# Optimization experiments

Measured on AMD Instinct MI355X. Metric: run time of the kernel, lower is better.

## Reference

```python
import jax, jax.numpy as jnp
import numpy as np

B, D, SL, N, H, LL = 2, 128, 1024, 64, 4, 4
LN_EPS = 1e-5
DIST_EPS = 1e-8


def _ln(x, g, b):
    m = x.mean(-1, keepdims=True)
    v = ((x - m) ** 2).mean(-1, keepdims=True)
    return (x - m) / jnp.sqrt(v + LN_EPS) * g + b


def _sla(x, qw, qb, kw, kb, vw, vb, ow, ob):
    # x: [B, R, C, D]; rank-1 scaled linear attention (head_qk_dim = 1)
    Bq, R, C, Dd = x.shape
    Hh = qw.shape[0]
    hd = Dd // Hh
    q = jnp.einsum('brcd,hd->brhc', x, qw) + qb[:, None]   # [B,R,H,C]
    k = jnp.einsum('brcd,hd->brhc', x, kw) + kb[:, None]
    q = jax.nn.elu(q) + 1.0
    k = jax.nn.elu(k) + 1.0
    q = q / q.mean(-1, keepdims=True)
    k = k / k.sum(-1, keepdims=True)
    v = (jnp.einsum('brcd,ed->brce', x, vw) + vb).reshape(Bq, R, C, Hh, hd)
    v = v.transpose(0, 1, 3, 2, 4)                         # [B,R,H,C,hd]
    ktv = jnp.einsum('brhc,brhce->brhe', k, v)             # [B,R,H,hd]
    V = jnp.einsum('brhc,brhe->brche', q, ktv)             # [B,R,C,H,hd]
    V = V.reshape(Bq, R, C, Dd)
    return jnp.einsum('brcd,ed->brce', V, ow) + ob


def _forward(x, rq_w, rq_b, rk_w, rk_b, rv_w, rv_b, ro_w, ro_b,
             cq_w, cq_b, ck_w, ck_b, cv_w, cv_b, co_w, co_b,
             ln_r_g, ln_r_b, ln_c_g, ln_c_b, ln_f_g, ln_f_b,
             f1_w, f1_b, f2_w, f2_b):
    y = x.transpose(0, 2, 3, 1)   # [B, L, N, D] channels-last

    def layer(y, p):
        (rqw, rqb, rkw, rkb, rvw, rvb, row_, rob,
         cqw, cqb, ckw, ckb, cvw, cvb, cow, cob,
         lrg, lrb, lcg, lcb, lfg, lfb, f1w, f1b, f2w, f2b) = p
        # row attention: rows = L, cols = N
        y = y + _sla(_ln(y, lrg, lrb), rqw, rqb, rkw, rkb, rvw, rvb, row_, rob)
        # col attention: rows = N, cols = L
        hc = _ln(y, lcg, lcb).swapaxes(1, 2)
        y = y + _sla(hc, cqw, cqb, ckw, ckb, cvw, cvb, cow, cob).swapaxes(1, 2)
        # FFN (1x1 convs == pointwise linears)
        hf = _ln(y, lfg, lfb)
        hf = jax.nn.gelu(jnp.einsum('blnd,ed->blne', hf, f1w) + f1b, approximate=False)
        y = y + (jnp.einsum('blne,de->blnd', hf, f2w) + f2b)
        return y, None

    params = (rq_w, rq_b, rk_w, rk_b, rv_w, rv_b, ro_w, ro_b,
              cq_w, cq_b, ck_w, ck_b, cv_w, cv_b, co_w, co_b,
              ln_r_g, ln_r_b, ln_c_g, ln_c_b, ln_f_g, ln_f_b,
              f1_w, f1_b, f2_w, f2_b)
    y, _ = jax.lax.scan(layer, y, params)

    # Euclidean pairwise distance head (use_cls=False): mean over sites 1..L
    xb = y[:, 1:].mean(axis=1)                 # [B, N, D]
    i0, i1 = np.tril_indices(N, -1)            # lower=True, diff=True ordering
    diffs = xb[:, i0] - xb[:, i1]              # [B, n_pairs, D]
    return jnp.sqrt(jnp.sum(diffs * diffs, axis=-1) + DIST_EPS)


def setup_inputs() -> dict:
    key = jax.random.key(0)
    ks = jax.random.split(key, 12)
    s = 0.02
    z = lambda *sh: jnp.zeros(sh, jnp.float32)
    o = lambda *sh: jnp.ones(sh, jnp.float32)
    w = lambda k, sh: jax.random.normal(k, sh, jnp.float32) * s
    p = {'x': jax.random.normal(ks[0], (B, D, SL, N), jnp.float32)}
    p['rq_w'] = w(ks[1], (LL, H, D)); p['rq_b'] = z(LL, H)
    p['rk_w'] = w(ks[2], (LL, H, D)); p['rk_b'] = z(LL, H)
    p['rv_w'] = w(ks[3], (LL, D, D)); p['rv_b'] = z(LL, D)
    p['ro_w'] = w(ks[4], (LL, D, D)); p['ro_b'] = z(LL, D)
    p['cq_w'] = w(ks[5], (LL, H, D)); p['cq_b'] = z(LL, H)
    p['ck_w'] = w(ks[6], (LL, H, D)); p['ck_b'] = z(LL, H)
    p['cv_w'] = w(ks[7], (LL, D, D)); p['cv_b'] = z(LL, D)
    p['co_w'] = w(ks[8], (LL, D, D)); p['co_b'] = z(LL, D)
    p['ln_r_g'] = o(LL, D); p['ln_r_b'] = z(LL, D)
    p['ln_c_g'] = o(LL, D); p['ln_c_b'] = z(LL, D)
    p['ln_f_g'] = o(LL, D); p['ln_f_b'] = z(LL, D)
    p['f1_w'] = w(ks[9], (LL, 4 * D, D)); p['f1_b'] = z(LL, 4 * D)
    p['f2_w'] = w(ks[10], (LL, D, 4 * D)); p['f2_b'] = z(LL, D)
    return p


def reference(x, rq_w, rq_b, rk_w, rk_b, rv_w, rv_b, ro_w, ro_b,
              cq_w, cq_b, ck_w, ck_b, cv_w, cv_b, co_w, co_b,
              ln_r_g, ln_r_b, ln_c_g, ln_c_b, ln_f_g, ln_f_b,
              f1_w, f1_b, f2_w, f2_b):
    return _forward(x, rq_w, rq_b, rk_w, rk_b, rv_w, rv_b, ro_w, ro_b,
                    cq_w, cq_b, ck_w, ck_b, cv_w, cv_b, co_w, co_b,
                    ln_r_g, ln_r_b, ln_c_g, ln_c_b, ln_f_g, ln_f_b,
                    f1_w, f1_b, f2_w, f2_b)
```

## Files before the change

### kernel.cpp

```cpp
#include <hip/hip_runtime.h>
#include <math.h>

#define LCNT 4

typedef float f32x4 __attribute__((ext_vector_type(4)));
typedef short bf16x8 __attribute__((ext_vector_type(8)));
typedef unsigned int u32;

__device__ __forceinline__ ushort bfr(float x){
  unsigned int b = __float_as_uint(x);
  return (ushort)((b + 0x7FFFu + ((b>>16)&1u)) >> 16);
}
__device__ __forceinline__ unsigned int pk2(float a, float b){
  return (unsigned int)bfr(a) | ((unsigned int)bfr(b)<<16);
}
__device__ __forceinline__ float fast_gelu(float v){
  float s = fabsf(v) * 0.70710678118f;
  float t = 1.0f/(1.0f + 0.3275911f*s);
  float p = t*(0.254829592f + t*(-0.284496736f + t*(1.421413741f +
            t*(-1.453152027f + t*1.061405429f))));
  float e = 1.0f - p*__expf(-s*s);
  e = copysignf(e, v);
  return 0.5f*v*(1.0f + e);
}
__device__ __forceinline__ void gl_lds16(const void* g, void* l){
  __builtin_amdgcn_global_load_lds(
      (const __attribute__((address_space(1))) u32*)g,
      (__attribute__((address_space(3))) u32*)l, 16, 0, 0);
}

__global__ __launch_bounds__(256) void k_transpose(const float* __restrict__ x,
                                                   float* __restrict__ y){
  int g = blockIdx.x;
  int b = g >> 10, l = g & 1023;
  __shared__ float sh[128*65];
  for (int idx = threadIdx.x; idx < 128*64; idx += 256){
    int d = idx >> 6, n = idx & 63;
    sh[d*65+n] = x[(((size_t)b*128 + d)*1024 + l)*64 + n];
  }
  __syncthreads();
  for (int idx = threadIdx.x; idx < 128*64; idx += 256){
    int n = idx >> 7, d = idx & 127;
    y[((size_t)g*64 + n)*128 + d] = sh[d*65+n];
  }
}

__global__ __launch_bounds__(256) void k_cvt(const float* __restrict__ src,
                                             ushort* __restrict__ dst, int n4){
  int i = blockIdx.x*256 + threadIdx.x;
  if (i < n4){
    float4 v = ((const float4*)src)[i];
    ushort4 p; p.x=bfr(v.x); p.y=bfr(v.y); p.z=bfr(v.z); p.w=bfr(v.w);
    ((ushort4*)dst)[i] = p;
  }
}

__global__ __launch_bounds__(256) void k_row(
    float* __restrict__ y,
    const float* __restrict__ rqw, const float* __restrict__ rqb,
    const float* __restrict__ rkw, const float* __restrict__ rkb,
    const float* __restrict__ rvw, const float* __restrict__ rvb,
    const float* __restrict__ roW, const float* __restrict__ rob,
    const float* __restrict__ lrg, const float* __restrict__ lrb,
    const float* __restrict__ cqw, const float* __restrict__ cqb,
    const float* __restrict__ ckw, const float* __restrict__ ckb,
    const float* __restrict__ lcg, const float* __restrict__ lcb,
    float2* __restrict__ stats,
    float* __restrict__ qout, float* __restrict__ kout)
{
  int g = blockIdx.x; int b = g>>10, l = g&1023;
  __shared__ float sh_h[64*129];
  __shared__ float sh_w4[2048];
  __shared__ float sh_q[256], sh_k[256];
  __shared__ float sh_hk[512];
  __shared__ float sh_ktv[128];
  __shared__ __align__(16) float sh_P[512];
  int tid = threadIdx.x;
  for (int i = tid; i < 512; i += 256){
    sh_w4[i] = rqw[i]; sh_w4[512+i] = rkw[i];
    sh_w4[1024+i] = cqw[i]; sh_w4[1536+i] = ckw[i];
  }
  int ttk = tid>>2, s4 = tid&3;
  float* yr = y + ((size_t)g*64 + ttk)*128 + s4*32;
  float4 v[8];
  #pragma unroll
  for (int i=0;i<8;i++) v[i] = *(const float4*)(yr + i*4);
  float sum = 0.f;
  #pragma unroll
  for (int i=0;i<8;i++) sum += v[i].x+v[i].y+v[i].z+v[i].w;
  sum += __shfl_xor(sum,1); sum += __shfl_xor(sum,2);
  float mean = sum*(1.0f/128.0f);
  float vs = 0.f;
  #pragma unroll
  for (int i=0;i<8;i++){
    v[i].x-=mean; v[i].y-=mean; v[i].z-=mean; v[i].w-=mean;
    vs += v[i].x*v[i].x+v[i].y*v[i].y+v[i].z*v[i].z+v[i].w*v[i].w;
  }
  vs += __shfl_xor(vs,1); vs += __shfl_xor(vs,2);
  float rstd = rsqrtf(vs*(1.0f/128.0f) + 1e-5f);
  {
    const float* gp = lrg + s4*32; const float* bp = lrb + s4*32;
    float* hrow = &sh_h[ttk*129 + s4*32];
    #pragma unroll
    for (int i=0;i<8;i++){
      float4 g4 = *(const float4*)(gp+i*4);
      float4 b4 = *(const float4*)(bp+i*4);
      hrow[i*4+0]=v[i].x*rstd*g4.x+b4.x;
      hrow[i*4+1]=v[i].y*rstd*g4.y+b4.y;
      hrow[i*4+2]=v[i].z*rstd*g4.z+b4.z;
      hrow[i*4+3]=v[i].w*rstd*g4.w+b4.w;
    }
  }
  __syncthreads();
  int h = tid>>6, n = tid&63;
  {
    float qr = rqb[h], kr = rkb[h];
    const float* qwp = sh_w4 + h*128;
    const float* kwp = sh_w4 + 512 + h*128;
    const float* hp  = sh_h + n*129;
    #pragma unroll 4
    for (int d=0; d<128; d++){ float hv=hp[d]; qr+=hv*qwp[d]; kr+=hv*kwp[d]; }
    qr = qr > 0.f ? qr + 1.f : __expf(qr);
    kr = kr > 0.f ? kr + 1.f : __expf(kr);
    float qs = qr; for (int m=32;m>=1;m>>=1) qs += __shfl_xor(qs, m);
    float ks = kr; for (int m=32;m>=1;m>>=1) ks += __shfl_xor(ks, m);
    sh_q[h*64+n] = qr * (64.f/qs);
    sh_k[h*64+n] = kr * (1.f/ks);
  }
  __syncthreads();
  #pragma unroll
  for (int r=0;r<2;r++){
    int idx = tid + r*256;
    int hh = idx>>7, d = idx&127;
    float acc = 0.f;
    #pragma unroll 4
    for (int nn=0;nn<64;nn++) acc += sh_k[hh*64+nn]*sh_h[nn*129+d];
    sh_hk[hh*128+d] = acc;
  }
  __syncthreads();
  if (tid < 128){
    float acc = rvb[tid];
    const float* vr = rvw + (size_t)tid*128;
    const float* hp2 = sh_hk + (tid>>5)*128;
    #pragma unroll 4
    for (int d=0;d<128;d++) acc += vr[d]*hp2[d];
    sh_ktv[tid] = acc;
  }
  __syncthreads();
  #pragma unroll
  for (int r=0;r<2;r++){
    int idx = tid + r*256;
    int hh = idx>>7, e = idx&127;
    float acc = 0.f;
    const float* orow = roW + (size_t)e*128 + hh*32;
    #pragma unroll 4
    for (int j=0;j<32;j++) acc += orow[j]*sh_ktv[hh*32+j];
    sh_P[hh*128+e] = acc;
  }
  __syncthreads();
  {
    float q0=sh_q[ttk], q1=sh_q[64+ttk], q2=sh_q[128+ttk], q3=sh_q[192+ttk];
    const float4* P4 = (const float4*)sh_P;
    #pragma unroll
    for (int i=0;i<8;i++){
      int d4 = s4*8 + i;
      float4 p0=P4[d4], p1=P4[32+d4], p2=P4[64+d4], p3=P4[96+d4];
      float4 o4=*(const float4*)&rob[s4*32+i*4];
      v[i].x += mean + o4.x + q0*p0.x+q1*p1.x+q2*p2.x+q3*p3.x;
      v[i].y += mean + o4.y + q0*p0.y+q1*p1.y+q2*p2.y+q3*p3.y;
      v[i].z += mean + o4.z + q0*p0.z+q1*p1.z+q2*p2.z+q3*p3.z;
      v[i].w += mean + o4.w + q0*p0.w+q1*p1.w+q2*p2.w+q3*p3.w;
      *(float4*)(yr + i*4) = v[i];
    }
  }
  float sum2 = 0.f;
  #pragma unroll
  for (int i=0;i<8;i++) sum2 += v[i].x+v[i].y+v[i].z+v[i].w;
  sum2 += __shfl_xor(sum2,1); sum2 += __shfl_xor(sum2,2);
  float cmean = sum2*(1.0f/128.0f);
  float cvs = 0.f;
  #pragma unroll
  for (int i=0;i<8;i++){
    v[i].x-=cmean; v[i].y-=cmean; v[i].z-=cmean; v[i].w-=cmean;
    cvs += v[i].x*v[i].x+v[i].y*v[i].y+v[i].z*v[i].z+v[i].w*v[i].w;
  }
  cvs += __shfl_xor(cvs,1); cvs += __shfl_xor(cvs,2);
  float crstd = rsqrtf(cvs*(1.0f/128.0f) + 1e-5f);
  if (s4 == 0) stats[(size_t)g*64 + ttk] = make_float2(cmean, crstd);
  {
    const float* gp = lcg + s4*32; const float* bp = lcb + s4*32;
    float* hrow = &sh_h[ttk*129 + s4*32];
    #pragma unroll
    for (int i=0;i<8;i++){
      float4 g4 = *(const float4*)(gp+i*4);
      float4 b4 = *(const float4*)(bp+i*4);
      hrow[i*4+0]=v[i].x*crstd*g4.x+b4.x;
      hrow[i*4+1]=v[i].y*crstd*g4.y+b4.y;
      hrow[i*4+2]=v[i].z*crstd*g4.z+b4.z;
      hrow[i*4+3]=v[i].w*crstd*g4.w+b4.w;
    }
  }
  __syncthreads();
  {
    float qv = cqb[h], kv = ckb[h];
    const float* qwp = sh_w4 + 1024 + h*128;
    const float* kwp = sh_w4 + 1536 + h*128;
    const float* hp  = sh_h + n*129;
    #pragma unroll 4
    for (int d=0; d<128; d++){ float hv=hp[d]; qv+=hv*qwp[d]; kv+=hv*kwp[d]; }
    qv = qv > 0.f ? qv + 1.f : __expf(qv);
    kv = kv > 0.f ? kv + 1.f : __expf(kv);
    size_t o = (((size_t)b*64 + n)*4 + h)*1024 + l;
    qout[o] = qv; kout[o] = kv;
  }
}

__global__ __launch_bounds__(256) void k_col_sum(const float* __restrict__ qin,
                                                 float* __restrict__ qs){
  int gg = blockIdx.x;
  const float* qp = qin + (size_t)gg*1024;
  float sq = 0.f;
  for (int i = threadIdx.x; i < 1024; i += 256) sq += qp[i];
  for (int m=32;m>=1;m>>=1) sq += __shfl_xor(sq, m);
  __shared__ float aq[4];
  int w = threadIdx.x >> 6;
  if ((threadIdx.x & 63) == 0) aq[w] = sq;
  __syncthreads();
  if (threadIdx.x == 0) qs[gg] = 1024.f/(aq[0]+aq[1]+aq[2]+aq[3]);
}

__global__ __launch_bounds__(256) void k_col_s1(
    const float* __restrict__ y, const float2* __restrict__ stats,
    const float* __restrict__ kin,
    float* __restrict__ s1p, float* __restrict__ Ab, float* __restrict__ Bb)
{
  int gg = blockIdx.x;
  int s = gg & 7, n = (gg>>3) & 63, b = gg>>9;
  int tid = threadIdx.x;
  int li = tid>>7, d = tid&127;
  const float* kp = kin + ((size_t)(b*64+n)*4)*1024;
  float a0=0.f,a1=0.f,a2=0.f,a3=0.f;
  float A0=0.f,A1=0.f,A2=0.f,A3=0.f;
  float B0=0.f,B1=0.f,B2=0.f,B3=0.f;
  for (int j=0;j<64;j++){
    int l = s*128 + 2*j + li;
    size_t t = ((size_t)(b*1024+l)*64+n);
    float2 st = stats[t];
    float w = st.y * y[t*128 + d];
    float rm = st.y*st.x;
    float k0 = kp[l], k1 = kp[1024+l], k2 = kp[2048+l], k3 = kp[3072+l];
    a0 += k0*w; a1 += k1*w; a2 += k2*w; a3 += k3*w;
    A0 += k0; A1 += k1; A2 += k2; A3 += k3;
    B0 += k0*rm; B1 += k1*rm; B2 += k2*rm; B3 += k3*rm;
  }
  __shared__ float shr[512];
  __shared__ float sAB[8];
  if (li == 1){
    shr[0*128+d]=a0; shr[1*128+d]=a1; shr[2*128+d]=a2; shr[3*128+d]=a3;
    if (d==0){ sAB[0]=A0; sAB[1]=A1; sAB[2]=A2; sAB[3]=A3;
               sAB[4]=B0; sAB[5]=B1; sAB[6]=B2; sAB[7]=B3; }
  }
  __syncthreads();
  if (li == 0){
    float* out = s1p + (size_t)gg*512;
    out[0*128+d] = a0 + shr[0*128+d];
    out[1*128+d] = a1 + shr[1*128+d];
    out[2*128+d] = a2 + shr[2*128+d];
    out[3*128+d] = a3 + shr[3*128+d];
    if (d==0){
      Ab[gg*4+0]=A0+sAB[0]; Ab[gg*4+1]=A1+sAB[1];
      Ab[gg*4+2]=A2+sAB[2]; Ab[gg*4+3]=A3+sAB[3];
      Bb[gg*4+0]=B0+sAB[4]; Bb[gg*4+1]=B1+sAB[5];
      Bb[gg*4+2]=B2+sAB[6]; Bb[gg*4+3]=B3+sAB[7];
    }
  }
}

__global__ __launch_bounds__(256) void k_col_ktvP(
    const float* __restrict__ s1p,
    const float* __restrict__ Ab, const float* __restrict__ Bb,
    const float* __restrict__ vw, const float* __restrict__ vb,
    const float* __restrict__ ow, const float* __restrict__ qsn,
    const float* __restrict__ lcg, const float* __restrict__ lcb,
    float* __restrict__ Pout)
{
  int gg = blockIdx.x;
  __shared__ float sh_hk[512];
  __shared__ float sh_ktv[128];
  __shared__ float sh_A[4], sh_B[4];
  int tid = threadIdx.x;
  #pragma unroll
  for (int r = 0; r < 2; r++){
    int idx = tid + r*256;
    float acc = 0.f;
    #pragma unroll
    for (int s = 0; s < 8; s++) acc += s1p[((size_t)gg*8 + s)*512 + idx];
    sh_hk[idx] = acc;
  }
  if (tid < 4){
    float a=0.f, bb=0.f;
    #pragma unroll
    for (int s = 0; s < 8; s++){ a += Ab[(gg*8+s)*4+tid]; bb += Bb[(gg*8+s)*4+tid]; }
    sh_A[tid]=a; sh_B[tid]=bb;
  }
  __syncthreads();
  #pragma unroll
  for (int r = 0; r < 2; r++){
    int idx = tid + r*256;
    int h = idx>>7, d = idx&127;
    float Ah = sh_A[h];
    sh_hk[idx] = lcg[d]*((sh_hk[idx]-sh_B[h])/Ah) + lcb[d];
  }
  __syncthreads();
  if (tid < 128){
    float acc = vb[tid];
    const float* vr = vw + (size_t)tid*128;
    const float* hp2 = sh_hk + (tid>>5)*128;
    #pragma unroll 4
    for (int d = 0; d < 128; d++) acc += vr[d]*hp2[d];
    sh_ktv[tid] = acc;
  }
  __syncthreads();
  #pragma unroll
  for (int r = 0; r < 2; r++){
    int idx = tid + r*256;
    int hh = idx >> 7, e = idx & 127;
    float acc = 0.f;
    const float* orow = ow + (size_t)e*128 + hh*32;
    #pragma unroll 4
    for (int j = 0; j < 32; j++) acc += orow[j]*sh_ktv[hh*32+j];
    Pout[(size_t)gg*512 + hh*128 + e] = acc * qsn[gg*4 + hh];
  }
}

__global__ __launch_bounds__(512, 4) void k_ffn(
    float* __restrict__ y,
    const float* __restrict__ qbuf, const float* __restrict__ Pb,
    const float* __restrict__ cob,
    const float* __restrict__ gam, const float* __restrict__ bet,
    const ushort* __restrict__ w1b, const float* __restrict__ b1,
    const ushort* __restrict__ w2b, const float* __restrict__ b2)
{
  __shared__ __align__(16) ushort pool[29952];
  ushort* sW1 = pool;
  ushort* sW2 = pool + 8192;
  ushort* sH  = pool + 16384;
  ushort* sHf = pool + 25088;
  float*  sF  = (float*)pool;
  int tid = threadIdx.x;
  int g = blockIdx.x; int b = g>>10, l = g&1023;
  size_t tb = (size_t)g*64;

  int wid = tid>>6, ln = tid&63;
  int lr = ln&15, gq = ln>>4;
  int wt = wid>>1, we = wid&1;
  int t0 = wt*16;

  #pragma unroll
  for (int i = 0; i < 2; i++){
    int row = wid*8 + i*4 + (ln>>4);
    gl_lds16(w1b + (size_t)row*128 + (((ln&15) ^ (row&7))<<3),
             &sW1[(wid*8 + i*4)*128]);
  }
  #pragma unroll
  for (int i = 0; i < 2; i++){
    int row = wid*16 + i*8 + (ln>>3);
    gl_lds16(w2b + (size_t)row*512 + (((ln&7) ^ (row&7))<<3),
             &sW2[(wid*16 + i*8)*64]);
  }

  int ttk = tid>>3, s8 = tid&7;
  float* yr = y + (tb+ttk)*128 + s8*16;
  float4 v[4];
  float fmean;
  {
    #pragma unroll
    for (int i = 0; i < 4; i++) v[i] = *(const float4*)(yr + i*4);
    const float* qp = qbuf + ((size_t)(b*64+ttk)*4)*1024 + l;
    float q0 = qp[0], q1 = qp[1024], q2 = qp[2048], q3 = qp[3072];
    const float* pr = Pb + (size_t)(b*64+ttk)*512 + s8*16;
    #pragma unroll
    for (int i = 0; i < 4; i++){
      float4 p0 = *(const float4*)(pr + i*4);
      float4 p1 = *(const float4*)(pr + 128 + i*4);
      float4 p2 = *(const float4*)(pr + 256 + i*4);
      float4 p3 = *(const float4*)(pr + 384 + i*4);
      float4 c4 = *(const float4*)&cob[s8*16 + i*4];
      v[i].x += c4.x + q0*p0.x+q1*p1.x+q2*p2.x+q3*p3.x;
      v[i].y += c4.y + q0*p0.y+q1*p1.y+q2*p2.y+q3*p3.y;
      v[i].z += c4.z + q0*p0.z+q1*p1.z+q2*p2.z+q3*p3.z;
      v[i].w += c4.w + q0*p0.w+q1*p1.w+q2*p2.w+q3*p3.w;
    }
    float sum = 0.f;
    #pragma unroll
    for (int i = 0; i < 4; i++) sum += v[i].x+v[i].y+v[i].z+v[i].w;
    sum += __shfl_xor(sum,1); sum += __shfl_xor(sum,2); sum += __shfl_xor(sum,4);
    fmean = sum*(1.0f/128.0f);
    float vs = 0.f;
    #pragma unroll
    for (int i = 0; i < 4; i++){
      v[i].x-=fmean; v[i].y-=fmean; v[i].z-=fmean; v[i].w-=fmean;
      vs += v[i].x*v[i].x+v[i].y*v[i].y+v[i].z*v[i].z+v[i].w*v[i].w;
    }
    vs += __shfl_xor(vs,1); vs += __shfl_xor(vs,2); vs += __shfl_xor(vs,4);
    float rstd = rsqrtf(vs*(1.0f/128.0f) + 1e-5f);
    const float* gp = gam + s8*16; const float* bp = bet + s8*16;
    #pragma unroll
    for (int i = 0; i < 2; i++){
      float4 ga = *(const float4*)(gp + i*8),     gb = *(const float4*)(gp + i*8 + 4);
      float4 ba = *(const float4*)(bp + i*8),     bb = *(const float4*)(bp + i*8 + 4);
      float4 va = v[i*2], vb2 = v[i*2+1];
      int4 o;
      o.x = (int)pk2(va.x*rstd*ga.x+ba.x,  va.y*rstd*ga.y+ba.y);
      o.y = (int)pk2(va.z*rstd*ga.z+ba.z,  va.w*rstd*ga.w+ba.w);
      o.z = (int)pk2(vb2.x*rstd*gb.x+bb.x, vb2.y*rstd*gb.y+bb.y);
      o.w = (int)pk2(vb2.z*rstd*gb.z+bb.z, vb2.w*rstd*gb.w+bb.w);
      *(int4*)&sH[ttk*136 + s8*16 + i*8] = o;
    }
  }
  __syncthreads();

  f32x4 acc2[4] = {};

  for (int c = 0; c < 8; c++){
    f32x4 acc1[2] = {};
    #pragma unroll
    for (int ks = 0; ks < 4; ks++){
      bf16x8 bfv = *(const bf16x8*)&sH[(t0+lr)*136 + ks*32 + gq*8];
      #pragma unroll
      for (int i = 0; i < 2; i++){
        int er = we*32 + i*16 + lr;
        bf16x8 afv = *(const bf16x8*)&sW1[er*128 + ((((ks<<2)|gq) ^ (lr&7))<<3)];
        acc1[i] = __builtin_amdgcn_mfma_f32_16x16x32_bf16(afv, bfv, acc1[i], 0, 0, 0);
      }
    }
    #pragma unroll
    for (int i = 0; i < 2; i++){
      float4 bb = *(const float4*)&b1[c*64 + we*32 + i*16 + gq*4];
      ushort4 pk;
      pk.x = bfr(fast_gelu(acc1[i][0] + bb.x));
      pk.y = bfr(fast_gelu(acc1[i][1] + bb.y));
      pk.z = bfr(fast_gelu(acc1[i][2] + bb.z));
      pk.w = bfr(fast_gelu(acc1[i][3] + bb.w));
      *(ushort4*)&sHf[(t0+lr)*72 + we*32 + i*16 + gq*4] = pk;
    }
    __syncthreads();
    if (c < 7){
      #pragma unroll
      for (int i = 0; i < 2; i++){
        int row = wid*8 + i*4 + (ln>>4);
        gl_lds16(w1b + (size_t)(c+1)*8192 + (size_t)row*128 + (((ln&15) ^ (row&7))<<3),
                 &sW1[(wid*8 + i*4)*128]);
      }
    }
    #pragma unroll
    for (int ks = 0; ks < 2; ks++){
      bf16x8 bfv = *(const bf16x8*)&sHf[(t0+lr)*72 + ks*32 + gq*8];
      #pragma unroll
      for (int j = 0; j < 4; j++){
        int dr = we*64 + j*16 + lr;
        bf16x8 afv = *(const bf16x8*)&sW2[dr*64 + ((((ks<<2)|gq) ^ (lr&7))<<3)];
        acc2[j] = __builtin_amdgcn_mfma_f32_16x16x32_bf16(afv, bfv, acc2[j], 0, 0, 0);
      }
    }
    __syncthreads();
    if (c < 7){
      #pragma unroll
      for (int i = 0; i < 2; i++){
        int row = wid*16 + i*8 + (ln>>3);
        gl_lds16(w2b + (size_t)row*512 + (c+1)*64 + (((ln&7) ^ (row&7))<<3),
                 &sW2[(wid*16 + i*8)*64]);
      }
    }
  }

  #pragma unroll
  for (int j = 0; j < 4; j++){
    float4 fo; fo.x=acc2[j][0]; fo.y=acc2[j][1]; fo.z=acc2[j][2]; fo.w=acc2[j][3];
    *(float4*)&sF[(t0+lr)*132 + we*64 + j*16 + gq*4] = fo;
  }
  __syncthreads();
  #pragma unroll
  for (int i = 0; i < 4; i++){
    float4 f = *(const float4*)&sF[ttk*132 + s8*16 + i*4];
    float4 b4 = *(const float4*)&b2[s8*16 + i*4];
    float4 o;
    o.x = v[i].x + fmean + f.x + b4.x;
    o.y = v[i].y + fmean + f.y + b4.y;
    o.z = v[i].z + fmean + f.z + b4.z;
    o.w = v[i].w + fmean + f.w + b4.w;
    *(float4*)(yr + i*4) = o;
  }
}

__global__ __launch_bounds__(128) void k_xbp(const float* __restrict__ y,
                                             float* __restrict__ xbq){
  int gg = blockIdx.x;
  int s = gg & 3, n = (gg>>2) & 63, b = gg>>8;
  int d = threadIdx.x;
  float acc = 0.f;
  int l0 = s*256 + (s==0 ? 1 : 0);
  const float* p = y + (((size_t)b*1024 + l0)*64 + n)*128 + d;
  for (int l = l0; l < s*256+256; l++){ acc += *p; p += 64*128; }
  xbq[(size_t)gg*128 + d] = acc;
}
__global__ __launch_bounds__(128) void k_xbr(const float* __restrict__ xbq,
                                             float* __restrict__ xb){
  int gg = blockIdx.x;
  int d = threadIdx.x;
  const float* q = xbq + (size_t)gg*512;
  xb[(size_t)gg*128 + d] = (q[d] + q[128+d] + q[256+d] + q[384+d]) * (1.0f/1023.0f);
}

__global__ __launch_bounds__(64) void k_dist(const float* __restrict__ xb,
                                             float* __restrict__ out){
  int p = blockIdx.x;
  int b = p >= 2016 ? 1 : 0;
  int pr = p - b*2016;
  int i0 = (int)((1.0f + sqrtf(1.0f + 8.0f*(float)pr))*0.5f);
  while (i0*(i0-1)/2 > pr) i0--;
  while ((i0+1)*i0/2 <= pr) i0++;
  int i1 = pr - i0*(i0-1)/2;
  int lane = threadIdx.x;
  const float* xa = xb + ((size_t)b*64 + i0)*128;
  const float* xc = xb + ((size_t)b*64 + i1)*128;
  float d0 = xa[lane]-xc[lane], d1 = xa[lane+64]-xc[lane+64];
  float s = d0*d0 + d1*d1;
  for (int m=32;m>=1;m>>=1) s += __shfl_xor(s, m);
  if (lane == 0) out[p] = sqrtf(s + 1e-8f);
}

extern "C" void kernel_launch(void* const* d_in, const int* in_sizes, int n_in,
                              void* d_out, int out_size, void* d_ws, size_t ws_size,
                              hipStream_t stream){
  const float* x    = (const float*)d_in[0];
  const float* rq_w = (const float*)d_in[1];  const float* rq_b = (const float*)d_in[2];
  const float* rk_w = (const float*)d_in[3];  const float* rk_b = (const float*)d_in[4];
  const float* rv_w = (const float*)d_in[5];  const float* rv_b = (const float*)d_in[6];
  const float* ro_w = (const float*)d_in[7];  const float* ro_b = (const float*)d_in[8];
  const float* cq_w = (const float*)d_in[9];  const float* cq_b = (const float*)d_in[10];
  const float* ck_w = (const float*)d_in[11]; const float* ck_b = (const float*)d_in[12];
  const float* cv_w = (const float*)d_in[13]; const float* cv_b = (const float*)d_in[14];
  const float* co_w = (const float*)d_in[15]; const float* co_b = (const float*)d_in[16];
  const float* lrg  = (const float*)d_in[17]; const float* lrb  = (const float*)d_in[18];
  const float* lcg  = (const float*)d_in[19]; const float* lcb  = (const float*)d_in[20];
  const float* lfg  = (const float*)d_in[21]; const float* lfb  = (const float*)d_in[22];
  const float* f1w  = (const float*)d_in[23]; const float* f1b  = (const float*)d_in[24];
  const float* f2w  = (const float*)d_in[25]; const float* f2b  = (const float*)d_in[26];

  float* ws = (float*)d_ws;
  float*  y   = ws;
  float2* st  = (float2*)(ws + 16777216);
  float*  qb_ = ws + 17039360;
  float*  kb_ = ws + 17563648;
  float*  Pb  = ws + 18087936;
  float*  s1p = ws + 19136512;
  float*  qs  = ws + 19660800;
  float*  xb  = ws + 19661824;
  ushort* w1b = (ushort*)(ws + 19678208);
  ushort* w2b = (ushort*)(ws + 19809280);
  float*  xbq = ws + 19940352;
  float*  Ab  = ws + 20005888;
  float*  Bb  = ws + 20009984;

  k_transpose<<<dim3(2048), dim3(256), 0, stream>>>(x, y);
  k_cvt<<<dim3(256), dim3(256), 0, stream>>>(f1w, w1b, 65536);
  k_cvt<<<dim3(256), dim3(256), 0, stream>>>(f2w, w2b, 65536);
  for (int l = 0; l < LCNT; l++){
    k_row<<<dim3(2048), dim3(256), 0, stream>>>(y,
        rq_w + l*512, rq_b + l*4, rk_w + l*512, rk_b + l*4,
        rv_w + (size_t)l*16384, rv_b + l*128, ro_w + (size_t)l*16384, ro_b + l*128,
        lrg + l*128, lrb + l*128,
        cq_w + l*512, cq_b + l*4, ck_w + l*512, ck_b + l*4,
        lcg + l*128, lcb + l*128,
        st, qb_, kb_);
    k_col_sum<<<dim3(512), dim3(256), 0, stream>>>(qb_, qs);
    k_col_s1<<<dim3(1024), dim3(256), 0, stream>>>(y, st, kb_, s1p, Ab, Bb);
    k_col_ktvP<<<dim3(128), dim3(256), 0, stream>>>(s1p, Ab, Bb,
        cv_w + (size_t)l*16384, cv_b + l*128, co_w + (size_t)l*16384, qs,
        lcg + l*128, lcb + l*128, Pb);
    k_ffn<<<dim3(2048), dim3(512), 0, stream>>>(y, qb_, Pb, co_b + l*128,
        lfg + l*128, lfb + l*128,
        w1b + (size_t)l*65536, f1b + l*512, w2b + (size_t)l*65536, f2b + l*128);
  }
  k_xbp<<<dim3(512), dim3(128), 0, stream>>>(y, xbq);
  k_xbr<<<dim3(128), dim3(128), 0, stream>>>(xbq, xb);
  k_dist<<<dim3(4032), dim3(64), 0, stream>>>(xb, (float*)d_out);
}
```

Baseline: 1.204 ms.

## Store q/k in token-major layout and replace erf GELU with sigmoid-tanh form

The column-attention q/k buffers are now stored per token as [b,l,h,n] instead of [b,n,h,l]. Writes from k_row become fully coalesced, and the consumers (k_col_s1, k_ffn) read the new layout. The q column sum is reorganised as a 16-block partial-sum kernel over the new layout, with the final reduction folded into k_col_ktvP. Separately, the erf-polynomial GELU is replaced by the tanh approximation written as x*sigmoid(...) using exp and rcp, which changes numerics away from exact GELU.

New measurement: 1.107 ms. 1.09x faster.

```diff
diff --git a/kernel.cpp b/kernel.cpp
--- a/kernel.cpp
+++ b/kernel.cpp
@@ -15,13 +15,10 @@
   return (unsigned int)bfr(a) | ((unsigned int)bfr(b)<<16);
 }
 __device__ __forceinline__ float fast_gelu(float v){
-  float s = fabsf(v) * 0.70710678118f;
-  float t = 1.0f/(1.0f + 0.3275911f*s);
-  float p = t*(0.254829592f + t*(-0.284496736f + t*(1.421413741f +
-            t*(-1.453152027f + t*1.061405429f))));
-  float e = 1.0f - p*__expf(-s*s);
-  e = copysignf(e, v);
-  return 0.5f*v*(1.0f + e);
+  float v2 = v*v;
+  float u = v*(-1.5957691f - 0.0713548162f*v2);
+  float e = __expf(u);
+  return v*__builtin_amdgcn_rcpf(1.f + e);
 }
 __device__ __forceinline__ void gl_lds16(const void* g, void* l){
   __builtin_amdgcn_global_load_lds(
@@ -68,7 +65,7 @@
     float2* __restrict__ stats,
     float* __restrict__ qout, float* __restrict__ kout)
 {
-  int g = blockIdx.x; int b = g>>10, l = g&1023;
+  int g = blockIdx.x;
   __shared__ float sh_h[64*129];
   __shared__ float sh_w4[2048];
   __shared__ float sh_q[256], sh_k[256];
@@ -210,23 +207,21 @@
     for (int d=0; d<128; d++){ float hv=hp[d]; qv+=hv*qwp[d]; kv+=hv*kwp[d]; }
     qv = qv > 0.f ? qv + 1.f : __expf(qv);
     kv = kv > 0.f ? kv + 1.f : __expf(kv);
-    size_t o = (((size_t)b*64 + n)*4 + h)*1024 + l;
+    size_t o = (size_t)g*256 + tid;
     qout[o] = qv; kout[o] = kv;
   }
 }
 
-__global__ __launch_bounds__(256) void k_col_sum(const float* __restrict__ qin,
-                                                 float* __restrict__ qs){
+__global__ __launch_bounds__(256) void k_qsum(const float* __restrict__ qin,
+                                              float* __restrict__ qsp){
   int gg = blockIdx.x;
-  const float* qp = qin + (size_t)gg*1024;
-  float sq = 0.f;
-  for (int i = threadIdx.x; i < 1024; i += 256) sq += qp[i];
-  for (int m=32;m>=1;m>>=1) sq += __shfl_xor(sq, m);
-  __shared__ float aq[4];
-  int w = threadIdx.x >> 6;
-  if ((threadIdx.x & 63) == 0) aq[w] = sq;
-  __syncthreads();
-  if (threadIdx.x == 0) qs[gg] = 1024.f/(aq[0]+aq[1]+aq[2]+aq[3]);
+  int c = gg&7, b = gg>>3;
+  int tid = threadIdx.x;
+  const float* qp = qin + ((size_t)b*1024 + c*128)*256 + tid;
+  float s = 0.f;
+  #pragma unroll 4
+  for (int j=0;j<128;j++){ s += *qp; qp += 256; }
+  qsp[(size_t)gg*256 + tid] = s;
 }
 
 __global__ __launch_bounds__(256) void k_col_s1(
@@ -238,7 +233,7 @@
   int s = gg & 7, n = (gg>>3) & 63, b = gg>>9;
   int tid = threadIdx.x;
   int li = tid>>7, d = tid&127;
-  const float* kp = kin + ((size_t)(b*64+n)*4)*1024;
+  const float* kp = kin + (size_t)b*262144 + n;
   float a0=0.f,a1=0.f,a2=0.f,a3=0.f;
   float A0=0.f,A1=0.f,A2=0.f,A3=0.f;
   float B0=0.f,B1=0.f,B2=0.f,B3=0.f;
@@ -248,7 +243,8 @@
     float2 st = stats[t];
     float w = st.y * y[t*128 + d];
     float rm = st.y*st.x;
-    float k0 = kp[l], k1 = kp[1024+l], k2 = kp[2048+l], k3 = kp[3072+l];
+    const float* kl = kp + (size_t)l*256;
+    float k0 = kl[0], k1 = kl[64], k2 = kl[128], k3 = kl[192];
     a0 += k0*w; a1 += k1*w; a2 += k2*w; a3 += k3*w;
     A0 += k0; A1 += k1; A2 += k2; A3 += k3;
     B0 += k0*rm; B1 += k1*rm; B2 += k2*rm; B3 += k3*rm;
@@ -279,15 +275,17 @@
 __global__ __launch_bounds__(256) void k_col_ktvP(
     const float* __restrict__ s1p,
     const float* __restrict__ Ab, const float* __restrict__ Bb,
+    const float* __restrict__ qsp,
     const float* __restrict__ vw, const float* __restrict__ vb,
-    const float* __restrict__ ow, const float* __restrict__ qsn,
+    const float* __restrict__ ow,
     const float* __restrict__ lcg, const float* __restrict__ lcb,
     float* __restrict__ Pout)
 {
   int gg = blockIdx.x;
+  int b = gg>>6, n = gg&63;
   __shared__ float sh_hk[512];
   __shared__ float sh_ktv[128];
-  __shared__ float sh_A[4], sh_B[4];
+  __shared__ float sh_A[4], sh_B[4], sh_qs[4];
   int tid = threadIdx.x;
   #pragma unroll
   for (int r = 0; r < 2; r++){
@@ -298,18 +296,19 @@
     sh_hk[idx] = acc;
   }
   if (tid < 4){
-    float a=0.f, bb=0.f;
+    float a=0.f, bb=0.f, q=0.f;
     #pragma unroll
     for (int s = 0; s < 8; s++){ a += Ab[(gg*8+s)*4+tid]; bb += Bb[(gg*8+s)*4+tid]; }
-    sh_A[tid]=a; sh_B[tid]=bb;
+    #pragma unroll
+    for (int c = 0; c < 8; c++) q += qsp[((b*8+c)<<8) + (tid<<6) + n];
+    sh_A[tid]=a; sh_B[tid]=bb; sh_qs[tid] = 1024.f/q;
   }
   __syncthreads();
   #pragma unroll
   for (int r = 0; r < 2; r++){
     int idx = tid + r*256;
     int h = idx>>7, d = idx&127;
-    float Ah = sh_A[h];
-    sh_hk[idx] = lcg[d]*((sh_hk[idx]-sh_B[h])/Ah) + lcb[d];
+    sh_hk[idx] = lcg[d]*((sh_hk[idx]-sh_B[h])/sh_A[h]) + lcb[d];
   }
   __syncthreads();
   if (tid < 128){
@@ -329,7 +328,7 @@
     const float* orow = ow + (size_t)e*128 + hh*32;
     #pragma unroll 4
     for (int j = 0; j < 32; j++) acc += orow[j]*sh_ktv[hh*32+j];
-    Pout[(size_t)gg*512 + hh*128 + e] = acc * qsn[gg*4 + hh];
+    Pout[(size_t)gg*512 + hh*128 + e] = acc * sh_qs[hh];
   }
 }
 
@@ -348,7 +347,7 @@
   ushort* sHf = pool + 25088;
   float*  sF  = (float*)pool;
   int tid = threadIdx.x;
-  int g = blockIdx.x; int b = g>>10, l = g&1023;
+  int g = blockIdx.x;
   size_t tb = (size_t)g*64;
 
   int wid = tid>>6, ln = tid&63;
@@ -376,9 +375,9 @@
   {
     #pragma unroll
     for (int i = 0; i < 4; i++) v[i] = *(const float4*)(yr + i*4);
-    const float* qp = qbuf + ((size_t)(b*64+ttk)*4)*1024 + l;
-    float q0 = qp[0], q1 = qp[1024], q2 = qp[2048], q3 = qp[3072];
-    const float* pr = Pb + (size_t)(b*64+ttk)*512 + s8*16;
+    const float* qp = qbuf + (size_t)g*256 + ttk;
+    float q0 = qp[0], q1 = qp[64], q2 = qp[128], q3 = qp[192];
+    const float* pr = Pb + ((size_t)((g>>10)*64 + ttk))*512 + s8*16;
     #pragma unroll
     for (int i = 0; i < 4; i++){
       float4 p0 = *(const float4*)(pr + i*4);
@@ -555,13 +554,13 @@
   float*  kb_ = ws + 17563648;
   float*  Pb  = ws + 18087936;
   float*  s1p = ws + 19136512;
-  float*  qs  = ws + 19660800;
   float*  xb  = ws + 19661824;
   ushort* w1b = (ushort*)(ws + 19678208);
   ushort* w2b = (ushort*)(ws + 19809280);
   float*  xbq = ws + 19940352;
   float*  Ab  = ws + 20005888;
   float*  Bb  = ws + 20009984;
+  float*  qsp = ws + 20014080;
 
   k_transpose<<<dim3(2048), dim3(256), 0, stream>>>(x, y);
   k_cvt<<<dim3(256), dim3(256), 0, stream>>>(f1w, w1b, 65536);
@@ -574,10 +573,10 @@
         cq_w + l*512, cq_b + l*4, ck_w + l*512, ck_b + l*4,
         lcg + l*128, lcb + l*128,
         st, qb_, kb_);
-    k_col_sum<<<dim3(512), dim3(256), 0, stream>>>(qb_, qs);
+    k_qsum<<<dim3(16), dim3(256), 0, stream>>>(qb_, qsp);
     k_col_s1<<<dim3(1024), dim3(256), 0, stream>>>(y, st, kb_, s1p, Ab, Bb);
-    k_col_ktvP<<<dim3(128), dim3(256), 0, stream>>>(s1p, Ab, Bb,
-        cv_w + (size_t)l*16384, cv_b + l*128, co_w + (size_t)l*16384, qs,
+    k_col_ktvP<<<dim3(128), dim3(256), 0, stream>>>(s1p, Ab, Bb, qsp,
+        cv_w + (size_t)l*16384, cv_b + l*128, co_w + (size_t)l*16384,
         lcg + l*128, lcb + l*128, Pb);
     k_ffn<<<dim3(2048), dim3(512), 0, stream>>>(y, qb_, Pb, co_b + l*128,
         lfg + l*128, lfb + l*128,
```
